# Optimization experiments

Measured on AMD Instinct MI355X. Metric: run time of the kernel, lower is better.

The kernel has to match this reference:

```python
import jax, jax.numpy as jnp
import numpy as np

B, S, EMB, HID, IMG, ATT, K, HL = 64, 512, 768, 512, 2048, 512, 6, 20


def setup_inputs() -> dict:
    key = jax.random.key(0)
    ks = jax.random.split(key, 14)
    u = lambda k, shape: jax.random.uniform(k, shape, jnp.float32, -0.1, 0.1)
    return {
        "representations": jax.random.normal(ks[0], (B, S, EMB), jnp.float32),
        "lengths": jax.random.randint(ks[1], (B,), 0, S),
        "separate_images": jax.random.normal(ks[2], (B, K, IMG), jnp.float32),
        "visual_context": jax.random.normal(ks[3], (B, K * IMG), jnp.float32),
        "prev_hist": jax.random.normal(ks[4], (B, K, HL, EMB), jnp.float32),
        "hist_counts": jax.random.randint(ks[5], (B, K), 0, HL + 1),
        "masks": jax.random.randint(ks[6], (B, S, 1), 0, 2).astype(bool),
        "W_sep": u(ks[7], (IMG, HID)), "b_sep": jnp.zeros((HID,), jnp.float32),
        "W_e2h": u(ks[8], (EMB, HID)), "b_e2h": jnp.zeros((HID,), jnp.float32),
        "W_hist": u(ks[9], (EMB, HID)), "b_hist": jnp.zeros((HID,), jnp.float32),
        "W_ctx": u(ks[10], (K * IMG, HID)), "b_ctx": jnp.zeros((HID,), jnp.float32),
        "W_mm": u(ks[11], (2 * HID, HID)), "b_mm": jnp.zeros((HID,), jnp.float32),
        "W_a1": u(ks[12], (HID, ATT)), "b_a1": jnp.zeros((ATT,), jnp.float32),
        "W_a2": u(ks[13], (ATT, 1)), "b_a2": jnp.zeros((1,), jnp.float32),
    }


def reference(representations, lengths, separate_images, visual_context,
              prev_hist, hist_counts, masks,
              W_sep, b_sep, W_e2h, b_e2h, W_hist, b_hist, W_ctx, b_ctx,
              W_mm, b_mm, W_a1, b_a1, W_a2, b_a2):
    # dropout_prob = 0 -> dropout is identity (eval-mode equivalence)
    input_reps = jax.nn.relu(representations @ W_e2h + b_e2h)          # [B,S,H]
    ctx = jax.nn.relu(visual_context @ W_ctx + b_ctx)                  # [B,H]
    ctx_rep = jnp.broadcast_to(ctx[:, None, :], input_reps.shape)
    mm = jax.nn.relu(jnp.concatenate([input_reps, ctx_rep], -1) @ W_mm + b_mm)  # [B,S,H]
    scores = jnp.tanh(mm @ W_a1 + b_a1) @ W_a2 + b_a2                  # [B,S,1]
    scores = jnp.where(masks, -jnp.inf, scores)
    att_w = jax.nn.softmax(scores, axis=1)                             # softmax over seq
    attended = jnp.sum(mm * att_w, axis=1)                             # [B,H]

    sep = separate_images @ W_sep + b_sep                              # [B,K,H]
    hl = prev_hist.shape[2]
    valid = jnp.arange(hl)[None, None, :] < hist_counts[:, :, None]    # [B,K,HL]
    hsum = jnp.sum(prev_hist * valid[..., None].astype(prev_hist.dtype), axis=2)
    havg = hsum / jnp.maximum(hist_counts, 1)[..., None].astype(prev_hist.dtype)
    hproj = jax.nn.relu(havg @ W_hist + b_hist)                        # [B,K,H]
    sep = sep + jnp.where((hist_counts > 0)[..., None], hproj, 0.0)
    sep = jax.nn.relu(sep)
    # F.normalize(p=2, dim=2, eps=1e-12)
    sep = sep / jnp.maximum(jnp.linalg.norm(sep, axis=2, keepdims=True), 1e-12)
    dot = jnp.einsum('bkh,bh->bk', sep, attended)[..., None]           # [B,K,1]
    return dot
```

## Files before the change

### kernel.cpp

```cpp
#include <hip/hip_runtime.h>
#include <math.h>

#define B_    64
#define S_    512
#define EMB_  768
#define HID_  512
#define IMG_  2048
#define ATT_  512
#define K_    6
#define HL_   20
#define MS_   (B_ * S_)

typedef __attribute__((ext_vector_type(8))) short bf16x8;
typedef __attribute__((ext_vector_type(4))) float f32x4;

__device__ __forceinline__ unsigned short f2b(float f) {
    unsigned int u = __float_as_uint(f);
    u += 0x7fffu + ((u >> 16) & 1u);
    return (unsigned short)(u >> 16);
}
__device__ __forceinline__ unsigned int pk_bf16(float lo, float hi) {
    unsigned int r;
    asm volatile("v_cvt_pk_bf16_f32 %0, %1, %2" : "=v"(r) : "v"(lo), "v"(hi));
    return r;
}

#define GLD_LDS16(gp, lp)                                                        \
    __builtin_amdgcn_global_load_lds(                                            \
        (const __attribute__((address_space(1))) void*)(gp),                     \
        (__attribute__((address_space(3))) void*)(lp), 16, 0, 0)

__global__ __launch_bounds__(256)
void prep(const float* __restrict__ W_e2h, const float* __restrict__ W_mm,
          const float* __restrict__ W_a1,
          unsigned short* __restrict__ WtE2H, unsigned short* __restrict__ WtMM,
          unsigned short* __restrict__ WtA1,
          const unsigned char* __restrict__ masks, int* __restrict__ flag) {
    const int z = blockIdx.z;
    if (z == 3) {
        if (blockIdx.x != 0 || blockIdx.y != 0) return;
        __shared__ int found;
        if (threadIdx.x == 0) found = 0;
        __syncthreads();
        for (int i = threadIdx.x; i < 8192; i += 256)
            if ((i & 3) != 0 && masks[i] != 0) found = 1;
        __syncthreads();
        if (threadIdx.x == 0) *flag = found;
        return;
    }
    const float* W;
    unsigned short* Wt;
    int Kd;
    if (z == 0)      { W = W_e2h; Wt = WtE2H; Kd = EMB_; }
    else if (z == 1) { W = W_mm;  Wt = WtMM;  Kd = HID_; }
    else             { W = W_a1;  Wt = WtA1;  Kd = HID_; }
    if ((int)blockIdx.x * 32 >= Kd) return;

    __shared__ float tile[32][33];
    int k0 = blockIdx.x * 32, n0 = blockIdx.y * 32;
    int tx = threadIdx.x & 31, ty = threadIdx.x >> 5;
    #pragma unroll
    for (int i = 0; i < 4; ++i)
        tile[ty + i * 8][tx] = W[(size_t)(k0 + ty + i * 8) * HID_ + n0 + tx];
    __syncthreads();
    #pragma unroll
    for (int i = 0; i < 4; ++i)
        Wt[(size_t)(n0 + ty + i * 8) * Kd + k0 + tx] = f2b(tile[tx][ty + i * 8]);
}

__device__ __forceinline__ void tile_coords(int N, int& bm, int& bn) {
    const int nwg = gridDim.x;
    const int cpx = nwg >> 3;
    const int lid = ((int)blockIdx.x & 7) * cpx + ((int)blockIdx.x >> 3);
    const int ntl = N >> 7;
    bn = (lid % ntl) << 7;
    bm = (lid / ntl) << 7;
}

template<bool AF32, int ACT, bool SCORE>
__global__ __launch_bounds__(256)
void gemm_pipe(const void* __restrict__ Av, const unsigned short* __restrict__ Bt,
               const float* __restrict__ bias, const float* __restrict__ row_add,
               int row_div, unsigned short* __restrict__ Co,
               const float* __restrict__ W_a2, float* __restrict__ scores8,
               int M, int N, int Kd) {
    __shared__ unsigned short Als[2][128 * 64];
    __shared__ unsigned short Bls[2][128 * 64];
    const int tid = threadIdx.x;
    int bm, bn; tile_coords(N, bm, bn);
    const int lane = tid & 63, wid = tid >> 6;
    const int wr = wid >> 1, wc = wid & 1;
    const int fr = lane & 15, hi = lane >> 4;

    const unsigned short* Ab = (const unsigned short*)Av;
    const float* Af = (const float*)Av;

    f32x4 acc[4][4] = {};
    int srow[4], lcol[4], scol[4];
    #pragma unroll
    for (int c = 0; c < 4; ++c) {
        int g = c * 256 + tid;
        srow[c] = g >> 3;
        lcol[c] = g & 7;
        scol[c] = lcol[c] ^ (srow[c] & 7);
    }

    float4 ra[8];

    auto stageA_lds = [&](int t, int buf) {
        #pragma unroll
        for (int c = 0; c < 4; ++c) {
            int g = c * 256 + tid;
            GLD_LDS16(Ab + (size_t)(bm + srow[c]) * Kd + t * 64 + scol[c] * 8,
                      &Als[buf][g * 8]);
        }
    };
    auto stageB_lds = [&](int t, int buf) {
        #pragma unroll
        for (int c = 0; c < 4; ++c) {
            int g = c * 256 + tid;
            GLD_LDS16(Bt + (size_t)(bn + srow[c]) * Kd + t * 64 + scol[c] * 8,
                      &Bls[buf][g * 8]);
        }
    };
    auto loadA_regs = [&](int t) {
        #pragma unroll
        for (int c = 0; c < 4; ++c) {
            const float* p = Af + (size_t)(bm + srow[c]) * Kd + t * 64 + lcol[c] * 8;
            ra[2 * c]     = *(const float4*)p;
            ra[2 * c + 1] = *(const float4*)(p + 4);
        }
    };
    auto writeA = [&](int buf) {
        #pragma unroll
        for (int c = 0; c < 4; ++c) {
            uint4 u;
            u.x = pk_bf16(ra[2*c].x,   ra[2*c].y);
            u.y = pk_bf16(ra[2*c].z,   ra[2*c].w);
            u.z = pk_bf16(ra[2*c+1].x, ra[2*c+1].y);
            u.w = pk_bf16(ra[2*c+1].z, ra[2*c+1].w);
            *(uint4*)&Als[buf][(srow[c] * 8 + scol[c]) * 8] = u;
        }
    };
    auto compute = [&](int buf) {
        #pragma unroll
        for (int kk = 0; kk < 2; ++kk) {
            bf16x8 af[4], bv[4];
            #pragma unroll
            for (int m = 0; m < 4; ++m) {
                int row = wr * 64 + m * 16 + fr;
                int sc = (kk * 4 + hi) ^ (fr & 7);
                af[m] = *(const bf16x8*)&Als[buf][row * 64 + sc * 8];
            }
            #pragma unroll
            for (int n = 0; n < 4; ++n) {
                int row = wc * 64 + n * 16 + fr;
                int sc = (kk * 4 + hi) ^ (fr & 7);
                bv[n] = *(const bf16x8*)&Bls[buf][row * 64 + sc * 8];
            }
            #pragma unroll
            for (int m = 0; m < 4; ++m)
                #pragma unroll
                for (int n = 0; n < 4; ++n)
                    acc[m][n] = __builtin_amdgcn_mfma_f32_16x16x32_bf16(af[m], bv[n], acc[m][n], 0, 0, 0);
        }
    };

    const int nt = Kd >> 6;

    if constexpr (AF32) {
        loadA_regs(0);
        stageB_lds(0, 0);
        writeA(0);
    } else {
        stageA_lds(0, 0);
        stageB_lds(0, 0);
    }

    for (int t = 0; t < nt; ++t) {
        const int buf = t & 1;
        const bool pf = (t + 1 < nt);
        if (pf) {
            if constexpr (AF32) {
                loadA_regs(t + 1);
                stageB_lds(t + 1, buf ^ 1);
            } else {
                stageA_lds(t + 1, buf ^ 1);
                stageB_lds(t + 1, buf ^ 1);
            }
        }
        __builtin_amdgcn_sched_barrier(0);
        if (pf) {
            if constexpr (AF32) asm volatile("s_waitcnt vmcnt(12)" ::: "memory");
            else                asm volatile("s_waitcnt vmcnt(8)"  ::: "memory");
        } else {
            asm volatile("s_waitcnt vmcnt(0)" ::: "memory");
        }
        __builtin_amdgcn_s_barrier();
        __builtin_amdgcn_sched_barrier(0);

        compute(buf);

        if constexpr (AF32) {
            if (pf) {
                writeA(buf ^ 1);
                asm volatile("s_waitcnt lgkmcnt(0)" ::: "memory");
            }
        }
        __builtin_amdgcn_sched_barrier(0);
        __builtin_amdgcn_s_barrier();
    }

    if (SCORE) {
        float ba[4], wa[4];
        #pragma unroll
        for (int n = 0; n < 4; ++n) {
            int col = bn + wc * 64 + n * 16 + fr;
            ba[n] = bias[col];
            wa[n] = W_a2[col];
        }
        const int slot = (bn >> 7) * 2 + wc;
        #pragma unroll
        for (int m = 0; m < 4; ++m) {
            #pragma unroll
            for (int r = 0; r < 4; ++r) {
                float p = 0.f;
                #pragma unroll
                for (int n = 0; n < 4; ++n)
                    p += tanhf(acc[m][n][r] + ba[n]) * wa[n];
                p += __shfl_xor(p, 1, 64);
                p += __shfl_xor(p, 2, 64);
                p += __shfl_xor(p, 4, 64);
                p += __shfl_xor(p, 8, 64);
                if (fr == 0)
                    scores8[(size_t)slot * M + bm + wr * 64 + m * 16 + hi * 4 + r] = p;
            }
        }
    } else {
        #pragma unroll
        for (int m = 0; m < 4; ++m) {
            #pragma unroll
            for (int n = 0; n < 4; ++n) {
                int col = bn + wc * 64 + n * 16 + fr;
                float badd = bias ? bias[col] : 0.f;
                #pragma unroll
                for (int r = 0; r < 4; ++r) {
                    int row = bm + wr * 64 + m * 16 + hi * 4 + r;
                    float x = acc[m][n][r] + badd;
                    if (row_add) x += row_add[(size_t)(row / row_div) * N + col];
                    if (ACT == 1) x = fmaxf(x, 0.f);
                    Co[(size_t)row * N + col] = f2b(x);
                }
            }
        }
    }
}

__global__ __launch_bounds__(256)
void gemm_splitk(const float* __restrict__ A, const float* __restrict__ W,
                 float* __restrict__ P, int M, int N, int Kd, int kps) {
    __shared__ float As[16][68];
    __shared__ float Ws[16][64];
    const int tid = threadIdx.x;
    const int bm = blockIdx.y * 64, bn = blockIdx.x * 64;
    const int ks = blockIdx.z;
    const int tx = tid & 15, ty = tid >> 4;
    const int arow = tid >> 2, akq = tid & 3;
    const int wk = tid >> 4, wnq = tid & 15;

    float acc[4][4] = {};
    const int kbeg = ks * kps, kend = kbeg + kps;

    for (int k0 = kbeg; k0 < kend; k0 += 16) {
        float4 av = *(const float4*)&A[(size_t)(bm + arow) * Kd + k0 + akq * 4];
        float4 wv = *(const float4*)&W[(size_t)(k0 + wk) * N + bn + wnq * 4];
        As[akq * 4 + 0][arow] = av.x;
        As[akq * 4 + 1][arow] = av.y;
        As[akq * 4 + 2][arow] = av.z;
        As[akq * 4 + 3][arow] = av.w;
        *(float4*)&Ws[wk][wnq * 4] = wv;
        __syncthreads();
        #pragma unroll
        for (int kk = 0; kk < 16; ++kk) {
            float4 a4 = *(const float4*)&As[kk][ty * 4];
            float4 b4 = *(const float4*)&Ws[kk][tx * 4];
            float a_[4] = {a4.x, a4.y, a4.z, a4.w};
            float b_[4] = {b4.x, b4.y, b4.z, b4.w};
            #pragma unroll
            for (int i = 0; i < 4; ++i)
                #pragma unroll
                for (int j = 0; j < 4; ++j)
                    acc[i][j] += a_[i] * b_[j];
        }
        __syncthreads();
    }

    float* Pbase = P + (size_t)ks * M * N;
    #pragma unroll
    for (int i = 0; i < 4; ++i) {
        int row = bm + ty * 4 + i;
        float4 v = {acc[i][0], acc[i][1], acc[i][2], acc[i][3]};
        *(float4*)&Pbase[(size_t)row * N + bn + tx * 4] = v;
    }
}

template<int ACT>
__global__ __launch_bounds__(256)
void reduce_k(const float* __restrict__ P, const float* __restrict__ bias,
              float* __restrict__ C, int MN, int N, int nsplit) {
    int idx = blockIdx.x * 256 + threadIdx.x;
    if (idx >= MN) return;
    float s = 0.f;
    for (int z = 0; z < nsplit; ++z) s += P[(size_t)z * MN + idx];
    if (bias) s += bias[idx & (N - 1)];
    if (ACT == 1) s = fmaxf(s, 0.f);
    C[idx] = s;
}

__global__ __launch_bounds__(256)
void softmax8(const float* __restrict__ scores8, const float* __restrict__ b_a2,
              const void* __restrict__ masks_raw, const int* __restrict__ flag,
              float* __restrict__ attw) {
    int b = blockIdx.x, tid = threadIdx.x;
    bool isb = (*flag) != 0;
    const unsigned char* mb = (const unsigned char*)masks_raw;
    const int* mi = (const int*)masks_raw;
    int lane = tid & 63, wv = tid >> 6;
    __shared__ float red[4], red2[4];
    float bias = b_a2[0];

    float m = -INFINITY;
    for (int s = tid; s < S_; s += 256) {
        int idx = b * S_ + s;
        float v = bias;
        #pragma unroll
        for (int z = 0; z < 8; ++z) v += scores8[(size_t)z * MS_ + idx];
        bool mk = isb ? (mb[idx] != 0) : (mi[idx] != 0);
        v = mk ? -INFINITY : v;
        attw[idx] = v;
        m = fmaxf(m, v);
    }
    #pragma unroll
    for (int off = 32; off; off >>= 1) m = fmaxf(m, __shfl_down(m, off, 64));
    if (lane == 0) red[wv] = m;
    __syncthreads();
    if (tid == 0) red[0] = fmaxf(fmaxf(red[0], red[1]), fmaxf(red[2], red[3]));
    __syncthreads();
    float Mx = red[0];

    float sum = 0.f;
    for (int s = tid; s < S_; s += 256) {
        int idx = b * S_ + s;
        float e = expf(attw[idx] - Mx);
        attw[idx] = e;
        sum += e;
    }
    #pragma unroll
    for (int off = 32; off; off >>= 1) sum += __shfl_down(sum, off, 64);
    if (lane == 0) red2[wv] = sum;
    __syncthreads();
    if (tid == 0) red2[0] = red2[0] + red2[1] + red2[2] + red2[3];
    __syncthreads();
    float inv = 1.f / red2[0];
    for (int s = tid; s < S_; s += 256) attw[b * S_ + s] *= inv;
}

__global__ __launch_bounds__(256)
void attended4(const unsigned short* __restrict__ mm, const float* __restrict__ attw,
               float* __restrict__ att4) {
    int b = blockIdx.x;
    int h = blockIdx.y * 256 + threadIdx.x;
    int z = blockIdx.z;
    __shared__ float w[128];
    int s0 = z * 128;
    if (threadIdx.x < 128) w[threadIdx.x] = attw[b * S_ + s0 + threadIdx.x];
    __syncthreads();
    float acc = 0.f;
    for (int s = 0; s < 128; ++s)
        acc += __uint_as_float((unsigned int)mm[((size_t)b * S_ + s0 + s) * HID_ + h] << 16) * w[s];
    att4[((size_t)z * B_ + b) * HID_ + h] = acc;
}

__global__ __launch_bounds__(256)
void hist_avg(const float* __restrict__ ph, const int* __restrict__ hcnt,
              float* __restrict__ havg) {
    int bk = blockIdx.x;
    int cnt = hcnt[bk];
    float denom = (float)(cnt > 1 ? cnt : 1);
    const float* base = ph + (size_t)bk * HL_ * EMB_;
    for (int e = threadIdx.x; e < EMB_; e += 256) {
        float s = 0.f;
        for (int l = 0; l < cnt; ++l) s += base[l * EMB_ + e];
        havg[bk * EMB_ + e] = s / denom;
    }
}

__global__ __launch_bounds__(256)
void combine_all(const float* __restrict__ skA, const float* __restrict__ skB,
                 const float* __restrict__ b_hist, const float* __restrict__ b_sep,
                 const int* __restrict__ hcnt, const float* __restrict__ att4,
                 float* __restrict__ out) {
    const int MNA = B_ * K_ * HID_;
    int bk = blockIdx.x, tid = threadIdx.x;
    int b = bk / K_;
    int cnt = hcnt[bk];
    float sq = 0.f, dt = 0.f;
    #pragma unroll
    for (int i = 0; i < HID_ / 256; ++i) {
        int h = tid + i * 256;
        size_t idx = (size_t)bk * HID_ + h;
        float hp = b_hist[h];
        #pragma unroll
        for (int z = 0; z < 8; ++z) hp += skA[(size_t)z * MNA + idx];
        hp = fmaxf(hp, 0.f);
        float sp = b_sep[h];
        #pragma unroll
        for (int z = 0; z < 16; ++z) sp += skB[(size_t)z * MNA + idx];
        float v = sp + (cnt > 0 ? hp : 0.f);
        v = fmaxf(v, 0.f);
        float at = 0.f;
        #pragma unroll
        for (int z = 0; z < 4; ++z) at += att4[((size_t)z * B_ + b) * HID_ + h];
        sq += v * v;
        dt += v * at;
    }
    #pragma unroll
    for (int off = 32; off; off >>= 1) {
        sq += __shfl_down(sq, off, 64);
        dt += __shfl_down(dt, off, 64);
    }
    __shared__ float rs[4], rd[4];
    int lane = tid & 63, wv = tid >> 6;
    if (lane == 0) { rs[wv] = sq; rd[wv] = dt; }
    __syncthreads();
    if (tid == 0) {
        float Sq = rs[0] + rs[1] + rs[2] + rs[3];
        float Dt = rd[0] + rd[1] + rd[2] + rd[3];
        float norm = fmaxf(sqrtf(Sq), 1e-12f);
        out[bk] = Dt / norm;
    }
}

extern "C" void kernel_launch(void* const* d_in, const int* in_sizes, int n_in,
                              void* d_out, int out_size, void* d_ws, size_t ws_size,
                              hipStream_t stream) {
    const float* reps     = (const float*)d_in[0];
    const float* sep_imgs = (const float*)d_in[2];
    const float* vctx     = (const float*)d_in[3];
    const float* phist    = (const float*)d_in[4];
    const int*   hcnt     = (const int*)d_in[5];
    const void*  masks    = d_in[6];
    const float* W_sep = (const float*)d_in[7];
    const float* b_sep = (const float*)d_in[8];
    const float* W_e2h = (const float*)d_in[9];
    const float* b_e2h = (const float*)d_in[10];
    const float* W_hist = (const float*)d_in[11];
    const float* b_hist = (const float*)d_in[12];
    const float* W_ctx = (const float*)d_in[13];
    const float* b_ctx = (const float*)d_in[14];
    const float* W_mm = (const float*)d_in[15];
    const float* b_mm = (const float*)d_in[16];
    const float* W_a1 = (const float*)d_in[17];
    const float* b_a1 = (const float*)d_in[18];
    const float* W_a2 = (const float*)d_in[19];
    const float* b_a2 = (const float*)d_in[20];
    float* out = (float*)d_out;

    const size_t MS = (size_t)MS_;
    const int MNA = B_ * K_ * HID_;

    unsigned short* actA  = (unsigned short*)d_ws;
    unsigned short* actB  = actA + MS * HID_;
    unsigned short* WtE2H = actB + MS * HID_;
    unsigned short* WtMM  = WtE2H + (size_t)EMB_ * HID_;
    unsigned short* WtA1  = WtMM + (size_t)HID_ * HID_;
    float* skC    = (float*)(WtA1 + (size_t)HID_ * HID_);
    float* skA    = skC + (size_t)64 * B_ * HID_;
    float* skB    = skA + (size_t)8 * MNA;
    float* scores8 = skB + (size_t)16 * MNA;
    float* attw   = scores8 + 8 * MS;
    float* att4   = attw + MS;
    float* ctx    = att4 + (size_t)4 * B_ * HID_;
    float* ctx2   = ctx + B_ * HID_;
    float* havg   = ctx2 + B_ * HID_;
    int*   flag   = (int*)(havg + (size_t)B_ * K_ * EMB_);

    prep<<<dim3(EMB_ / 32, HID_ / 32, 4), 256, 0, stream>>>(
        W_e2h, W_mm, W_a1, WtE2H, WtMM, WtA1, (const unsigned char*)masks, flag);

    {
        const int nsp = 64, kps = (K_ * IMG_) / nsp;
        gemm_splitk<<<dim3(8, 1, nsp), 256, 0, stream>>>(vctx, W_ctx, skC,
                                                         B_, HID_, K_ * IMG_, kps);
        reduce_k<1><<<(B_ * HID_ + 255) / 256, 256, 0, stream>>>(skC, b_ctx, ctx,
                                                                 B_ * HID_, HID_, nsp);
    }
    {
        const int nsp = 8, kps = HID_ / nsp;
        gemm_splitk<<<dim3(8, 1, nsp), 256, 0, stream>>>(ctx, W_mm + (size_t)HID_ * HID_,
                                                         skC, B_, HID_, HID_, kps);
        reduce_k<0><<<(B_ * HID_ + 255) / 256, 256, 0, stream>>>(skC, b_mm, ctx2,
                                                                 B_ * HID_, HID_, nsp);
    }

    const int big_grid = (MS_ / 128) * (HID_ / 128);
    gemm_pipe<true, 1, false><<<big_grid, 256, 0, stream>>>(
        reps, WtE2H, b_e2h, nullptr, 1, actA, nullptr, nullptr, MS_, HID_, EMB_);
    gemm_pipe<false, 1, false><<<big_grid, 256, 0, stream>>>(
        actA, WtMM, nullptr, ctx2, S_, actB, nullptr, nullptr, MS_, HID_, HID_);
    gemm_pipe<false, 0, true><<<big_grid, 256, 0, stream>>>(
        actB, WtA1, b_a1, nullptr, 1, actA, W_a2, scores8, MS_, ATT_, HID_);
    softmax8<<<B_, 256, 0, stream>>>(scores8, b_a2, masks, flag, attw);
    attended4<<<dim3(B_, HID_ / 256, 4), 256, 0, stream>>>(actB, attw, att4);
    hist_avg<<<B_ * K_, 256, 0, stream>>>(phist, hcnt, havg);
    gemm_splitk<<<dim3(8, 6, 8), 256, 0, stream>>>(havg, W_hist, skA,
                                                   B_ * K_, HID_, EMB_, EMB_ / 8);
    gemm_splitk<<<dim3(8, 6, 16), 256, 0, stream>>>(sep_imgs, W_sep, skB,
                                                    B_ * K_, HID_, IMG_, IMG_ / 16);
    combine_all<<<B_ * K_, 256, 0, stream>>>(skA, skB, b_hist, b_sep, hcnt,
                                             att4, out);
}
```

Before: 261.3 us.

## Halve GEMM K-tile, deepen fp32 A prefetch, raise occupancy, vectorize attended

The pipelined GEMM now uses a 32-wide K tile instead of 64, which halves LDS use and lets the kernel declare a minimum of 4 blocks per SM, with a 4-way XOR swizzle replacing the 8-way one. For the fp32-A path it adds a second register buffer so A is prefetched two K-steps ahead, and it raises MFMA wave priority during compute. The attended kernel is changed so each thread reads two packed bf16 values per load and writes a float2, which halves the grid. The trade-off is twice as many barrier and K-loop iterations, plus possible register pressure from the extra prefetch buffer under the occupancy bound.

```diff
diff --git a/kernel.cpp b/kernel.cpp
--- a/kernel.cpp
+++ b/kernel.cpp
@@ -24,6 +24,7 @@
     asm volatile("v_cvt_pk_bf16_f32 %0, %1, %2" : "=v"(r) : "v"(lo), "v"(hi));
     return r;
 }
+__device__ __forceinline__ int swz4(int r) { return (r ^ (r >> 2)) & 3; }
 
 #define GLD_LDS16(gp, lp)                                                        \
     __builtin_amdgcn_global_load_lds(                                            \
@@ -78,14 +79,14 @@
 }
 
 template<bool AF32, int ACT, bool SCORE>
-__global__ __launch_bounds__(256)
+__global__ __launch_bounds__(256, 4)
 void gemm_pipe(const void* __restrict__ Av, const unsigned short* __restrict__ Bt,
                const float* __restrict__ bias, const float* __restrict__ row_add,
                int row_div, unsigned short* __restrict__ Co,
                const float* __restrict__ W_a2, float* __restrict__ scores8,
                int M, int N, int Kd) {
-    __shared__ unsigned short Als[2][128 * 64];
-    __shared__ unsigned short Bls[2][128 * 64];
+    __shared__ unsigned short Als[2][128 * 32];
+    __shared__ unsigned short Bls[2][128 * 32];
     const int tid = threadIdx.x;
     int bm, bn; tile_coords(N, bm, bn);
     const int lane = tid & 63, wid = tid >> 6;
@@ -96,119 +97,120 @@
     const float* Af = (const float*)Av;
 
     f32x4 acc[4][4] = {};
-    int srow[4], lcol[4], scol[4];
-    #pragma unroll
-    for (int c = 0; c < 4; ++c) {
+    int srow[2], lin[2], scol[2];
+    #pragma unroll
+    for (int c = 0; c < 2; ++c) {
         int g = c * 256 + tid;
-        srow[c] = g >> 3;
-        lcol[c] = g & 7;
-        scol[c] = lcol[c] ^ (srow[c] & 7);
-    }
-
-    float4 ra[8];
+        srow[c] = g >> 2;
+        lin[c]  = g & 3;
+        scol[c] = lin[c] ^ swz4(srow[c]);
+    }
+
+    float4 raA[4], raB[4];
 
     auto stageA_lds = [&](int t, int buf) {
         #pragma unroll
-        for (int c = 0; c < 4; ++c) {
+        for (int c = 0; c < 2; ++c) {
             int g = c * 256 + tid;
-            GLD_LDS16(Ab + (size_t)(bm + srow[c]) * Kd + t * 64 + scol[c] * 8,
+            GLD_LDS16(Ab + (size_t)(bm + srow[c]) * Kd + t * 32 + scol[c] * 8,
                       &Als[buf][g * 8]);
         }
     };
     auto stageB_lds = [&](int t, int buf) {
         #pragma unroll
-        for (int c = 0; c < 4; ++c) {
+        for (int c = 0; c < 2; ++c) {
             int g = c * 256 + tid;
-            GLD_LDS16(Bt + (size_t)(bn + srow[c]) * Kd + t * 64 + scol[c] * 8,
+            GLD_LDS16(Bt + (size_t)(bn + srow[c]) * Kd + t * 32 + scol[c] * 8,
                       &Bls[buf][g * 8]);
         }
     };
-    auto loadA_regs = [&](int t) {
-        #pragma unroll
-        for (int c = 0; c < 4; ++c) {
-            const float* p = Af + (size_t)(bm + srow[c]) * Kd + t * 64 + lcol[c] * 8;
+    auto loadA = [&](int t, float4 (&ra)[4]) {
+        #pragma unroll
+        for (int c = 0; c < 2; ++c) {
+            const float* p = Af + (size_t)(bm + srow[c]) * Kd + t * 32 + scol[c] * 8;
             ra[2 * c]     = *(const float4*)p;
             ra[2 * c + 1] = *(const float4*)(p + 4);
         }
     };
-    auto writeA = [&](int buf) {
-        #pragma unroll
-        for (int c = 0; c < 4; ++c) {
+    auto writeA = [&](float4 (&ra)[4], int buf) {
+        #pragma unroll
+        for (int c = 0; c < 2; ++c) {
             uint4 u;
             u.x = pk_bf16(ra[2*c].x,   ra[2*c].y);
             u.y = pk_bf16(ra[2*c].z,   ra[2*c].w);
             u.z = pk_bf16(ra[2*c+1].x, ra[2*c+1].y);
             u.w = pk_bf16(ra[2*c+1].z, ra[2*c+1].w);
-            *(uint4*)&Als[buf][(srow[c] * 8 + scol[c]) * 8] = u;
+            *(uint4*)&Als[buf][(srow[c] * 4 + lin[c]) * 8] = u;
         }
     };
     auto compute = [&](int buf) {
-        #pragma unroll
-        for (int kk = 0; kk < 2; ++kk) {
-            bf16x8 af[4], bv[4];
+        bf16x8 af[4], bv[4];
+        #pragma unroll
+        for (int m = 0; m < 4; ++m) {
+            int r = wr * 64 + m * 16 + fr;
+            af[m] = *(const bf16x8*)&Als[buf][r * 32 + (hi ^ swz4(r)) * 8];
+        }
+        #pragma unroll
+        for (int n = 0; n < 4; ++n) {
+            int r = wc * 64 + n * 16 + fr;
+            bv[n] = *(const bf16x8*)&Bls[buf][r * 32 + (hi ^ swz4(r)) * 8];
+        }
+        __builtin_amdgcn_s_setprio(1);
+        #pragma unroll
+        for (int m = 0; m < 4; ++m)
             #pragma unroll
-            for (int m = 0; m < 4; ++m) {
-                int row = wr * 64 + m * 16 + fr;
-                int sc = (kk * 4 + hi) ^ (fr & 7);
-                af[m] = *(const bf16x8*)&Als[buf][row * 64 + sc * 8];
-            }
-            #pragma unroll
-            for (int n = 0; n < 4; ++n) {
-                int row = wc * 64 + n * 16 + fr;
-                int sc = (kk * 4 + hi) ^ (fr & 7);
-                bv[n] = *(const bf16x8*)&Bls[buf][row * 64 + sc * 8];
-            }
-            #pragma unroll
-            for (int m = 0; m < 4; ++m)
-                #pragma unroll
-                for (int n = 0; n < 4; ++n)
-                    acc[m][n] = __builtin_amdgcn_mfma_f32_16x16x32_bf16(af[m], bv[n], acc[m][n], 0, 0, 0);
-        }
+            for (int n = 0; n < 4; ++n)
+                acc[m][n] = __builtin_amdgcn_mfma_f32_16x16x32_bf16(af[m], bv[n], acc[m][n], 0, 0, 0);
+        __builtin_amdgcn_s_setprio(0);
     };
 
-    const int nt = Kd >> 6;
+    const int nt = Kd >> 5;
 
     if constexpr (AF32) {
-        loadA_regs(0);
+        loadA(0, raA);
         stageB_lds(0, 0);
-        writeA(0);
+        writeA(raA, 0);
+        loadA(1, raB);
     } else {
         stageA_lds(0, 0);
         stageB_lds(0, 0);
     }
 
-    for (int t = 0; t < nt; ++t) {
-        const int buf = t & 1;
-        const bool pf = (t + 1 < nt);
-        if (pf) {
-            if constexpr (AF32) {
-                loadA_regs(t + 1);
-                stageB_lds(t + 1, buf ^ 1);
-            } else {
-                stageA_lds(t + 1, buf ^ 1);
-                stageB_lds(t + 1, buf ^ 1);
-            }
-        }
+    auto phase = [&](int u, float4 (&raPF)[4], float4 (&raWR)[4],
+                     int bufU, int bufN) {
+        const bool pf1 = (u + 1 < nt);
+        const bool pf2 = (u + 2 < nt);
+        if constexpr (AF32) {
+            if (pf2) loadA(u + 2, raPF);
+        } else {
+            if (pf1) stageA_lds(u + 1, bufN);
+        }
+        if (pf1) stageB_lds(u + 1, bufN);
         __builtin_amdgcn_sched_barrier(0);
-        if (pf) {
-            if constexpr (AF32) asm volatile("s_waitcnt vmcnt(12)" ::: "memory");
-            else                asm volatile("s_waitcnt vmcnt(8)"  ::: "memory");
+        if constexpr (AF32) {
+            if (pf2)      asm volatile("s_waitcnt vmcnt(6)" ::: "memory");
+            else if (pf1) asm volatile("s_waitcnt vmcnt(2)" ::: "memory");
+            else          asm volatile("s_waitcnt vmcnt(0)" ::: "memory");
         } else {
-            asm volatile("s_waitcnt vmcnt(0)" ::: "memory");
+            if (pf1) asm volatile("s_waitcnt vmcnt(4)" ::: "memory");
+            else     asm volatile("s_waitcnt vmcnt(0)" ::: "memory");
         }
         __builtin_amdgcn_s_barrier();
         __builtin_amdgcn_sched_barrier(0);
-
-        compute(buf);
-
+        compute(bufU);
         if constexpr (AF32) {
-            if (pf) {
-                writeA(buf ^ 1);
+            if (pf1) {
+                writeA(raWR, bufN);
                 asm volatile("s_waitcnt lgkmcnt(0)" ::: "memory");
             }
         }
         __builtin_amdgcn_sched_barrier(0);
         __builtin_amdgcn_s_barrier();
+    };
+
+    for (int u = 0; u < nt; u += 2) {
+        phase(u,     raA, raB, 0, 1);
+        phase(u + 1, raB, raA, 1, 0);
     }
 
     if (SCORE) {
@@ -368,17 +370,22 @@
 __global__ __launch_bounds__(256)
 void attended4(const unsigned short* __restrict__ mm, const float* __restrict__ attw,
                float* __restrict__ att4) {
-    int b = blockIdx.x;
-    int h = blockIdx.y * 256 + threadIdx.x;
-    int z = blockIdx.z;
+    int b = blockIdx.x, z = blockIdx.y;
+    int h2 = threadIdx.x;
     __shared__ float w[128];
     int s0 = z * 128;
     if (threadIdx.x < 128) w[threadIdx.x] = attw[b * S_ + s0 + threadIdx.x];
     __syncthreads();
-    float acc = 0.f;
-    for (int s = 0; s < 128; ++s)
-        acc += __uint_as_float((unsigned int)mm[((size_t)b * S_ + s0 + s) * HID_ + h] << 16) * w[s];
-    att4[((size_t)z * B_ + b) * HID_ + h] = acc;
+    const unsigned int* base =
+        (const unsigned int*)mm + ((size_t)b * S_ + s0) * (HID_ / 2) + h2;
+    float a0 = 0.f, a1 = 0.f;
+    for (int s = 0; s < 128; ++s) {
+        unsigned int u = base[(size_t)s * (HID_ / 2)];
+        a0 += __uint_as_float(u << 16) * w[s];
+        a1 += __uint_as_float(u & 0xffff0000u) * w[s];
+    }
+    float2 r = {a0, a1};
+    *(float2*)&att4[((size_t)z * B_ + b) * HID_ + h2 * 2] = r;
 }
 
 __global__ __launch_bounds__(256)
@@ -511,7 +518,7 @@
     gemm_pipe<false, 0, true><<<big_grid, 256, 0, stream>>>(
         actB, WtA1, b_a1, nullptr, 1, actA, W_a2, scores8, MS_, ATT_, HID_);
     softmax8<<<B_, 256, 0, stream>>>(scores8, b_a2, masks, flag, attw);
-    attended4<<<dim3(B_, HID_ / 256, 4), 256, 0, stream>>>(actB, attw, att4);
+    attended4<<<dim3(B_, 4), 256, 0, stream>>>(actB, attw, att4);
     hist_avg<<<B_ * K_, 256, 0, stream>>>(phist, hcnt, havg);
     gemm_splitk<<<dim3(8, 6, 8), 256, 0, stream>>>(havg, W_hist, skA,
                                                    B_ * K_, HID_, EMB_, EMB_ / 8);
```

Result: slower. 359.4 us (+37.6%).

## Merge independent GEMMs into horizontally fused mega-kernels and vectorize attended reduction

Applied to the files above, without the earlier changes.

Independent work (the e2h GEMM, the context split-K GEMM, the history averaging and the separate-image split-K GEMM) now runs inside one launch that dispatches on block index, and the mm GEMM is merged the same way with the W_hist split-K. The aim is to cut launch count and fill idle compute units during small GEMMs. The pipelined GEMM loses its hand-tuned vmcnt waits and sched barriers in favor of plain __syncthreads, which may serialize the load/compute overlap. attended4 now reads two bf16 values per 32-bit load, with one block covering all 512 columns.

```diff
diff --git a/kernel.cpp b/kernel.cpp
--- a/kernel.cpp
+++ b/kernel.cpp
@@ -68,26 +68,26 @@
         Wt[(size_t)(n0 + ty + i * 8) * Kd + k0 + tx] = f2b(tile[tx][ty + i * 8]);
 }
 
-__device__ __forceinline__ void tile_coords(int N, int& bm, int& bn) {
-    const int nwg = gridDim.x;
+__device__ __forceinline__ void tile_coords(int bid, int nwg, int N, int& bm, int& bn) {
     const int cpx = nwg >> 3;
-    const int lid = ((int)blockIdx.x & 7) * cpx + ((int)blockIdx.x >> 3);
+    const int lid = (bid & 7) * cpx + (bid >> 3);
     const int ntl = N >> 7;
     bn = (lid % ntl) << 7;
     bm = (lid / ntl) << 7;
 }
 
 template<bool AF32, int ACT, bool SCORE>
-__global__ __launch_bounds__(256)
-void gemm_pipe(const void* __restrict__ Av, const unsigned short* __restrict__ Bt,
+__device__ __forceinline__
+void gemm_body(unsigned char* smem, int bid, int nwg,
+               const void* __restrict__ Av, const unsigned short* __restrict__ Bt,
                const float* __restrict__ bias, const float* __restrict__ row_add,
                int row_div, unsigned short* __restrict__ Co,
                const float* __restrict__ W_a2, float* __restrict__ scores8,
                int M, int N, int Kd) {
-    __shared__ unsigned short Als[2][128 * 64];
-    __shared__ unsigned short Bls[2][128 * 64];
+    unsigned short* Als = (unsigned short*)smem;
+    unsigned short* Bls = Als + 2 * 128 * 64;
     const int tid = threadIdx.x;
-    int bm, bn; tile_coords(N, bm, bn);
+    int bm, bn; tile_coords(bid, nwg, N, bm, bn);
     const int lane = tid & 63, wid = tid >> 6;
     const int wr = wid >> 1, wc = wid & 1;
     const int fr = lane & 15, hi = lane >> 4;
@@ -112,7 +112,7 @@
         for (int c = 0; c < 4; ++c) {
             int g = c * 256 + tid;
             GLD_LDS16(Ab + (size_t)(bm + srow[c]) * Kd + t * 64 + scol[c] * 8,
-                      &Als[buf][g * 8]);
+                      &Als[buf * 8192 + g * 8]);
         }
     };
     auto stageB_lds = [&](int t, int buf) {
@@ -120,10 +120,10 @@
         for (int c = 0; c < 4; ++c) {
             int g = c * 256 + tid;
             GLD_LDS16(Bt + (size_t)(bn + srow[c]) * Kd + t * 64 + scol[c] * 8,
-                      &Bls[buf][g * 8]);
+                      &Bls[buf * 8192 + g * 8]);
         }
     };
-    auto loadA_regs = [&](int t) {
+    auto loadA = [&](int t) {
         #pragma unroll
         for (int c = 0; c < 4; ++c) {
             const float* p = Af + (size_t)(bm + srow[c]) * Kd + t * 64 + lcol[c] * 8;
@@ -139,7 +139,7 @@
             u.y = pk_bf16(ra[2*c].z,   ra[2*c].w);
             u.z = pk_bf16(ra[2*c+1].x, ra[2*c+1].y);
             u.w = pk_bf16(ra[2*c+1].z, ra[2*c+1].w);
-            *(uint4*)&Als[buf][(srow[c] * 8 + scol[c]) * 8] = u;
+            *(uint4*)&Als[buf * 8192 + (srow[c] * 8 + scol[c]) * 8] = u;
         }
     };
     auto compute = [&](int buf) {
@@ -148,15 +148,15 @@
             bf16x8 af[4], bv[4];
             #pragma unroll
             for (int m = 0; m < 4; ++m) {
-                int row = wr * 64 + m * 16 + fr;
+                int r = wr * 64 + m * 16 + fr;
                 int sc = (kk * 4 + hi) ^ (fr & 7);
-                af[m] = *(const bf16x8*)&Als[buf][row * 64 + sc * 8];
+                af[m] = *(const bf16x8*)&Als[buf * 8192 + r * 64 + sc * 8];
             }
             #pragma unroll
             for (int n = 0; n < 4; ++n) {
-                int row = wc * 64 + n * 16 + fr;
+                int r = wc * 64 + n * 16 + fr;
                 int sc = (kk * 4 + hi) ^ (fr & 7);
-                bv[n] = *(const bf16x8*)&Bls[buf][row * 64 + sc * 8];
+                bv[n] = *(const bf16x8*)&Bls[buf * 8192 + r * 64 + sc * 8];
             }
             #pragma unroll
             for (int m = 0; m < 4; ++m)
@@ -169,46 +169,32 @@
     const int nt = Kd >> 6;
 
     if constexpr (AF32) {
-        loadA_regs(0);
+        loadA(0);
         stageB_lds(0, 0);
         writeA(0);
     } else {
         stageA_lds(0, 0);
         stageB_lds(0, 0);
     }
+    __syncthreads();
 
     for (int t = 0; t < nt; ++t) {
         const int buf = t & 1;
         const bool pf = (t + 1 < nt);
         if (pf) {
             if constexpr (AF32) {
-                loadA_regs(t + 1);
+                loadA(t + 1);
                 stageB_lds(t + 1, buf ^ 1);
             } else {
                 stageA_lds(t + 1, buf ^ 1);
                 stageB_lds(t + 1, buf ^ 1);
             }
         }
-        __builtin_amdgcn_sched_barrier(0);
-        if (pf) {
-            if constexpr (AF32) asm volatile("s_waitcnt vmcnt(12)" ::: "memory");
-            else                asm volatile("s_waitcnt vmcnt(8)"  ::: "memory");
-        } else {
-            asm volatile("s_waitcnt vmcnt(0)" ::: "memory");
-        }
-        __builtin_amdgcn_s_barrier();
-        __builtin_amdgcn_sched_barrier(0);
-
         compute(buf);
-
         if constexpr (AF32) {
-            if (pf) {
-                writeA(buf ^ 1);
-                asm volatile("s_waitcnt lgkmcnt(0)" ::: "memory");
-            }
-        }
-        __builtin_amdgcn_sched_barrier(0);
-        __builtin_amdgcn_s_barrier();
+            if (pf) writeA(buf ^ 1);
+        }
+        __syncthreads();
     }
 
     if (SCORE) {
@@ -256,20 +242,20 @@
     }
 }
 
-__global__ __launch_bounds__(256)
-void gemm_splitk(const float* __restrict__ A, const float* __restrict__ W,
+__device__ __forceinline__
+void splitk_body(unsigned char* smem, int bx, int by, int bz,
+                 const float* __restrict__ A, const float* __restrict__ W,
                  float* __restrict__ P, int M, int N, int Kd, int kps) {
-    __shared__ float As[16][68];
-    __shared__ float Ws[16][64];
+    float (*As)[68] = (float(*)[68])smem;
+    float (*Ws)[64] = (float(*)[64])(smem + 16 * 68 * 4);
     const int tid = threadIdx.x;
-    const int bm = blockIdx.y * 64, bn = blockIdx.x * 64;
-    const int ks = blockIdx.z;
+    const int bm = by * 64, bn = bx * 64;
     const int tx = tid & 15, ty = tid >> 4;
     const int arow = tid >> 2, akq = tid & 3;
     const int wk = tid >> 4, wnq = tid & 15;
 
     float acc[4][4] = {};
-    const int kbeg = ks * kps, kend = kbeg + kps;
+    const int kbeg = bz * kps, kend = kbeg + kps;
 
     for (int k0 = kbeg; k0 < kend; k0 += 16) {
         float4 av = *(const float4*)&A[(size_t)(bm + arow) * Kd + k0 + akq * 4];
@@ -295,13 +281,86 @@
         __syncthreads();
     }
 
-    float* Pbase = P + (size_t)ks * M * N;
+    float* Pbase = P + (size_t)bz * M * N;
     #pragma unroll
     for (int i = 0; i < 4; ++i) {
         int row = bm + ty * 4 + i;
         float4 v = {acc[i][0], acc[i][1], acc[i][2], acc[i][3]};
         *(float4*)&Pbase[(size_t)row * N + bn + tx * 4] = v;
     }
+}
+
+__device__ __forceinline__
+void hist_body(const float* __restrict__ ph, const int* __restrict__ hcnt,
+               float* __restrict__ havg, int bk) {
+    int cnt = hcnt[bk];
+    float denom = (float)(cnt > 1 ? cnt : 1);
+    const float* base = ph + (size_t)bk * HL_ * EMB_;
+    for (int e = threadIdx.x; e < EMB_; e += 256) {
+        float s = 0.f;
+        for (int l = 0; l < cnt; ++l) s += base[l * EMB_ + e];
+        havg[bk * EMB_ + e] = s / denom;
+    }
+}
+
+__global__ __launch_bounds__(256)
+void mega1(const float* __restrict__ reps, const unsigned short* __restrict__ WtE2H,
+           const float* __restrict__ b_e2h, unsigned short* __restrict__ actA,
+           const float* __restrict__ vctx, const float* __restrict__ W_ctx,
+           float* __restrict__ skC,
+           const float* __restrict__ phist, const int* __restrict__ hcnt,
+           float* __restrict__ havg,
+           const float* __restrict__ sep_imgs, const float* __restrict__ W_sep,
+           float* __restrict__ skB) {
+    __shared__ __align__(16) unsigned char smem[65536];
+    const int bid = blockIdx.x;
+    if (bid < 1024) {
+        gemm_body<true, 1, false>(smem, bid, 1024, reps, WtE2H, b_e2h, nullptr, 1,
+                                  actA, nullptr, nullptr, MS_, HID_, EMB_);
+    } else if (bid < 1536) {
+        int b = bid - 1024;
+        splitk_body(smem, b & 7, 0, b >> 3, vctx, W_ctx, skC, B_, HID_,
+                    K_ * IMG_, (K_ * IMG_) / 64);
+    } else if (bid < 1920) {
+        hist_body(phist, hcnt, havg, bid - 1536);
+    } else {
+        int b = bid - 1920;
+        splitk_body(smem, b & 7, (b >> 3) % 6, b / 48, sep_imgs, W_sep, skB,
+                    B_ * K_, HID_, IMG_, IMG_ / 16);
+    }
+}
+
+__global__ __launch_bounds__(256)
+void mega2(const unsigned short* __restrict__ actA, const unsigned short* __restrict__ WtMM,
+           const float* __restrict__ ctx2, unsigned short* __restrict__ actB,
+           const float* __restrict__ havg, const float* __restrict__ W_hist,
+           float* __restrict__ skA) {
+    __shared__ __align__(16) unsigned char smem[65536];
+    const int bid = blockIdx.x;
+    if (bid < 1024) {
+        gemm_body<false, 1, false>(smem, bid, 1024, actA, WtMM, nullptr, ctx2, S_,
+                                   actB, nullptr, nullptr, MS_, HID_, HID_);
+    } else {
+        int b = bid - 1024;
+        splitk_body(smem, b & 7, (b >> 3) % 6, b / 48, havg, W_hist, skA,
+                    B_ * K_, HID_, EMB_, EMB_ / 8);
+    }
+}
+
+__global__ __launch_bounds__(256)
+void gemm_score(const unsigned short* __restrict__ actB, const unsigned short* __restrict__ WtA1,
+                const float* __restrict__ b_a1, const float* __restrict__ W_a2,
+                float* __restrict__ scores8) {
+    __shared__ __align__(16) unsigned char smem[65536];
+    gemm_body<false, 0, true>(smem, blockIdx.x, 1024, actB, WtA1, b_a1, nullptr, 1,
+                              nullptr, W_a2, scores8, MS_, ATT_, HID_);
+}
+
+__global__ __launch_bounds__(256)
+void gemm_splitk(const float* __restrict__ A, const float* __restrict__ W,
+                 float* __restrict__ P, int M, int N, int Kd, int kps) {
+    __shared__ __align__(16) unsigned char smem[16 * 68 * 4 + 16 * 64 * 4];
+    splitk_body(smem, blockIdx.x, blockIdx.y, blockIdx.z, A, W, P, M, N, Kd, kps);
 }
 
 template<int ACT>
@@ -368,31 +427,22 @@
 __global__ __launch_bounds__(256)
 void attended4(const unsigned short* __restrict__ mm, const float* __restrict__ attw,
                float* __restrict__ att4) {
-    int b = blockIdx.x;
-    int h = blockIdx.y * 256 + threadIdx.x;
-    int z = blockIdx.z;
+    int b = blockIdx.x, z = blockIdx.y;
+    int h2 = threadIdx.x;
     __shared__ float w[128];
     int s0 = z * 128;
     if (threadIdx.x < 128) w[threadIdx.x] = attw[b * S_ + s0 + threadIdx.x];
     __syncthreads();
-    float acc = 0.f;
-    for (int s = 0; s < 128; ++s)
-        acc += __uint_as_float((unsigned int)mm[((size_t)b * S_ + s0 + s) * HID_ + h] << 16) * w[s];
-    att4[((size_t)z * B_ + b) * HID_ + h] = acc;
-}
-
-__global__ __launch_bounds__(256)
-void hist_avg(const float* __restrict__ ph, const int* __restrict__ hcnt,
-              float* __restrict__ havg) {
-    int bk = blockIdx.x;
-    int cnt = hcnt[bk];
-    float denom = (float)(cnt > 1 ? cnt : 1);
-    const float* base = ph + (size_t)bk * HL_ * EMB_;
-    for (int e = threadIdx.x; e < EMB_; e += 256) {
-        float s = 0.f;
-        for (int l = 0; l < cnt; ++l) s += base[l * EMB_ + e];
-        havg[bk * EMB_ + e] = s / denom;
-    }
+    const unsigned int* base =
+        (const unsigned int*)mm + ((size_t)b * S_ + s0) * (HID_ / 2) + h2;
+    float a0 = 0.f, a1 = 0.f;
+    for (int s = 0; s < 128; ++s) {
+        unsigned int u = base[(size_t)s * (HID_ / 2)];
+        a0 += __uint_as_float(u << 16) * w[s];
+        a1 += __uint_as_float(u & 0xffff0000u) * w[s];
+    }
+    float2 r = {a0, a1};
+    *(float2*)&att4[((size_t)z * B_ + b) * HID_ + h2 * 2] = r;
 }
 
 __global__ __launch_bounds__(256)
@@ -488,35 +538,24 @@
     prep<<<dim3(EMB_ / 32, HID_ / 32, 4), 256, 0, stream>>>(
         W_e2h, W_mm, W_a1, WtE2H, WtMM, WtA1, (const unsigned char*)masks, flag);
 
-    {
-        const int nsp = 64, kps = (K_ * IMG_) / nsp;
-        gemm_splitk<<<dim3(8, 1, nsp), 256, 0, stream>>>(vctx, W_ctx, skC,
-                                                         B_, HID_, K_ * IMG_, kps);
-        reduce_k<1><<<(B_ * HID_ + 255) / 256, 256, 0, stream>>>(skC, b_ctx, ctx,
-                                                                 B_ * HID_, HID_, nsp);
-    }
-    {
-        const int nsp = 8, kps = HID_ / nsp;
-        gemm_splitk<<<dim3(8, 1, nsp), 256, 0, stream>>>(ctx, W_mm + (size_t)HID_ * HID_,
-                                                         skC, B_, HID_, HID_, kps);
-        reduce_k<0><<<(B_ * HID_ + 255) / 256, 256, 0, stream>>>(skC, b_mm, ctx2,
-                                                                 B_ * HID_, HID_, nsp);
-    }
-
-    const int big_grid = (MS_ / 128) * (HID_ / 128);
-    gemm_pipe<true, 1, false><<<big_grid, 256, 0, stream>>>(
-        reps, WtE2H, b_e2h, nullptr, 1, actA, nullptr, nullptr, MS_, HID_, EMB_);
-    gemm_pipe<false, 1, false><<<big_grid, 256, 0, stream>>>(
-        actA, WtMM, nullptr, ctx2, S_, actB, nullptr, nullptr, MS_, HID_, HID_);
-    gemm_pipe<false, 0, true><<<big_grid, 256, 0, stream>>>(
-        actB, WtA1, b_a1, nullptr, 1, actA, W_a2, scores8, MS_, ATT_, HID_);
+    mega1<<<2688, 256, 0, stream>>>(reps, WtE2H, b_e2h, actA,
+                                    vctx, W_ctx, skC,
+                                    phist, hcnt, havg,
+                                    sep_imgs, W_sep, skB);
+
+    reduce_k<1><<<(B_ * HID_ + 255) / 256, 256, 0, stream>>>(skC, b_ctx, ctx,
+                                                             B_ * HID_, HID_, 64);
+    gemm_splitk<<<dim3(8, 1, 8), 256, 0, stream>>>(ctx, W_mm + (size_t)HID_ * HID_,
+                                                   skC, B_, HID_, HID_, HID_ / 8);
+    reduce_k<0><<<(B_ * HID_ + 255) / 256, 256, 0, stream>>>(skC, b_mm, ctx2,
+                                                             B_ * HID_, HID_, 8);
+
+    mega2<<<1408, 256, 0, stream>>>(actA, WtMM, ctx2, actB, havg, W_hist, skA);
+
+    gemm_score<<<1024, 256, 0, stream>>>(actB, WtA1, b_a1, W_a2, scores8);
+
     softmax8<<<B_, 256, 0, stream>>>(scores8, b_a2, masks, flag, attw);
-    attended4<<<dim3(B_, HID_ / 256, 4), 256, 0, stream>>>(actB, attw, att4);
-    hist_avg<<<B_ * K_, 256, 0, stream>>>(phist, hcnt, havg);
-    gemm_splitk<<<dim3(8, 6, 8), 256, 0, stream>>>(havg, W_hist, skA,
-                                                   B_ * K_, HID_, EMB_, EMB_ / 8);
-    gemm_splitk<<<dim3(8, 6, 16), 256, 0, stream>>>(sep_imgs, W_sep, skB,
-                                                    B_ * K_, HID_, IMG_, IMG_ / 16);
+    attended4<<<dim3(B_, 4), 256, 0, stream>>>(actB, attw, att4);
     combine_all<<<B_ * K_, 256, 0, stream>>>(skA, skB, b_hist, b_sep, hcnt,
                                              att4, out);
 }
```

After: 303.7 us. +16.2%, slower.

## Enlarge main GEMM tiles to 256x256 with 512 threads; vectorize attended reduction

Applied to the files above, without the earlier changes.

Replaces the 128x128, 256-thread pipelined bf16 MFMA GEMM with a 256x256 tile run by 512 threads (8 waves in a 2x4 layout, 8x4 accumulator fragments per wave). The aim is more operand reuse per LDS load and less global traffic per output. The hand-tuned vmcnt waits and split barriers are replaced by a plain __syncthreads per K-step. This uses 128KB of LDS per block and leaves only 256 blocks, about one per CU, so overlap between loading and compute could suffer. The attended4 kernel now loads two bf16 values per 32-bit access and stores float2 results, halving its thread count.

```diff
diff --git a/kernel.cpp b/kernel.cpp
--- a/kernel.cpp
+++ b/kernel.cpp
@@ -68,38 +68,37 @@
         Wt[(size_t)(n0 + ty + i * 8) * Kd + k0 + tx] = f2b(tile[tx][ty + i * 8]);
 }
 
-__device__ __forceinline__ void tile_coords(int N, int& bm, int& bn) {
+template<bool AF32, int ACT, bool SCORE>
+__global__ __launch_bounds__(512)
+void gemm256(const void* __restrict__ Av, const unsigned short* __restrict__ Bt,
+             const float* __restrict__ bias, const float* __restrict__ row_add,
+             int row_div, unsigned short* __restrict__ Co,
+             const float* __restrict__ W_a2, float* __restrict__ scores8,
+             int M, int N, int Kd) {
+    __shared__ unsigned short Als[2][256 * 64];
+    __shared__ unsigned short Bls[2][256 * 64];
+    const int tid = threadIdx.x;
+
     const int nwg = gridDim.x;
     const int cpx = nwg >> 3;
     const int lid = ((int)blockIdx.x & 7) * cpx + ((int)blockIdx.x >> 3);
-    const int ntl = N >> 7;
-    bn = (lid % ntl) << 7;
-    bm = (lid / ntl) << 7;
-}
-
-template<bool AF32, int ACT, bool SCORE>
-__global__ __launch_bounds__(256)
-void gemm_pipe(const void* __restrict__ Av, const unsigned short* __restrict__ Bt,
-               const float* __restrict__ bias, const float* __restrict__ row_add,
-               int row_div, unsigned short* __restrict__ Co,
-               const float* __restrict__ W_a2, float* __restrict__ scores8,
-               int M, int N, int Kd) {
-    __shared__ unsigned short Als[2][128 * 64];
-    __shared__ unsigned short Bls[2][128 * 64];
-    const int tid = threadIdx.x;
-    int bm, bn; tile_coords(N, bm, bn);
+    const int ntl = N >> 8;
+    const int bn = (lid % ntl) << 8;
+    const int bm = (lid / ntl) << 8;
+
     const int lane = tid & 63, wid = tid >> 6;
-    const int wr = wid >> 1, wc = wid & 1;
+    const int wr = wid >> 2, wc = wid & 3;
     const int fr = lane & 15, hi = lane >> 4;
 
     const unsigned short* Ab = (const unsigned short*)Av;
     const float* Af = (const float*)Av;
 
-    f32x4 acc[4][4] = {};
+    f32x4 acc[8][4] = {};
+
     int srow[4], lcol[4], scol[4];
     #pragma unroll
     for (int c = 0; c < 4; ++c) {
-        int g = c * 256 + tid;
+        int g = c * 512 + tid;
         srow[c] = g >> 3;
         lcol[c] = g & 7;
         scol[c] = lcol[c] ^ (srow[c] & 7);
@@ -110,7 +109,7 @@
     auto stageA_lds = [&](int t, int buf) {
         #pragma unroll
         for (int c = 0; c < 4; ++c) {
-            int g = c * 256 + tid;
+            int g = c * 512 + tid;
             GLD_LDS16(Ab + (size_t)(bm + srow[c]) * Kd + t * 64 + scol[c] * 8,
                       &Als[buf][g * 8]);
         }
@@ -118,15 +117,15 @@
     auto stageB_lds = [&](int t, int buf) {
         #pragma unroll
         for (int c = 0; c < 4; ++c) {
-            int g = c * 256 + tid;
+            int g = c * 512 + tid;
             GLD_LDS16(Bt + (size_t)(bn + srow[c]) * Kd + t * 64 + scol[c] * 8,
                       &Bls[buf][g * 8]);
         }
     };
-    auto loadA_regs = [&](int t) {
+    auto loadA = [&](int t) {
         #pragma unroll
         for (int c = 0; c < 4; ++c) {
-            const float* p = Af + (size_t)(bm + srow[c]) * Kd + t * 64 + lcol[c] * 8;
+            const float* p = Af + (size_t)(bm + srow[c]) * Kd + t * 64 + scol[c] * 8;
             ra[2 * c]     = *(const float4*)p;
             ra[2 * c + 1] = *(const float4*)(p + 4);
         }
@@ -134,32 +133,33 @@
     auto writeA = [&](int buf) {
         #pragma unroll
         for (int c = 0; c < 4; ++c) {
+            int g = c * 512 + tid;
             uint4 u;
             u.x = pk_bf16(ra[2*c].x,   ra[2*c].y);
             u.y = pk_bf16(ra[2*c].z,   ra[2*c].w);
             u.z = pk_bf16(ra[2*c+1].x, ra[2*c+1].y);
             u.w = pk_bf16(ra[2*c+1].z, ra[2*c+1].w);
-            *(uint4*)&Als[buf][(srow[c] * 8 + scol[c]) * 8] = u;
+            *(uint4*)&Als[buf][g * 8] = u;
         }
     };
     auto compute = [&](int buf) {
         #pragma unroll
         for (int kk = 0; kk < 2; ++kk) {
-            bf16x8 af[4], bv[4];
+            bf16x8 af[8], bv[4];
             #pragma unroll
-            for (int m = 0; m < 4; ++m) {
-                int row = wr * 64 + m * 16 + fr;
-                int sc = (kk * 4 + hi) ^ (fr & 7);
-                af[m] = *(const bf16x8*)&Als[buf][row * 64 + sc * 8];
+            for (int m = 0; m < 8; ++m) {
+                int r = wr * 128 + m * 16 + fr;
+                int sc = (kk * 4 + hi) ^ (r & 7);
+                af[m] = *(const bf16x8*)&Als[buf][r * 64 + sc * 8];
             }
             #pragma unroll
             for (int n = 0; n < 4; ++n) {
-                int row = wc * 64 + n * 16 + fr;
-                int sc = (kk * 4 + hi) ^ (fr & 7);
-                bv[n] = *(const bf16x8*)&Bls[buf][row * 64 + sc * 8];
+                int r = wc * 64 + n * 16 + fr;
+                int sc = (kk * 4 + hi) ^ (r & 7);
+                bv[n] = *(const bf16x8*)&Bls[buf][r * 64 + sc * 8];
             }
             #pragma unroll
-            for (int m = 0; m < 4; ++m)
+            for (int m = 0; m < 8; ++m)
                 #pragma unroll
                 for (int n = 0; n < 4; ++n)
                     acc[m][n] = __builtin_amdgcn_mfma_f32_16x16x32_bf16(af[m], bv[n], acc[m][n], 0, 0, 0);
@@ -169,46 +169,32 @@
     const int nt = Kd >> 6;
 
     if constexpr (AF32) {
-        loadA_regs(0);
+        loadA(0);
         stageB_lds(0, 0);
         writeA(0);
     } else {
         stageA_lds(0, 0);
         stageB_lds(0, 0);
     }
+    __syncthreads();
 
     for (int t = 0; t < nt; ++t) {
         const int buf = t & 1;
         const bool pf = (t + 1 < nt);
         if (pf) {
             if constexpr (AF32) {
-                loadA_regs(t + 1);
+                loadA(t + 1);
                 stageB_lds(t + 1, buf ^ 1);
             } else {
                 stageA_lds(t + 1, buf ^ 1);
                 stageB_lds(t + 1, buf ^ 1);
             }
         }
-        __builtin_amdgcn_sched_barrier(0);
-        if (pf) {
-            if constexpr (AF32) asm volatile("s_waitcnt vmcnt(12)" ::: "memory");
-            else                asm volatile("s_waitcnt vmcnt(8)"  ::: "memory");
-        } else {
-            asm volatile("s_waitcnt vmcnt(0)" ::: "memory");
-        }
-        __builtin_amdgcn_s_barrier();
-        __builtin_amdgcn_sched_barrier(0);
-
         compute(buf);
-
         if constexpr (AF32) {
-            if (pf) {
-                writeA(buf ^ 1);
-                asm volatile("s_waitcnt lgkmcnt(0)" ::: "memory");
-            }
-        }
-        __builtin_amdgcn_sched_barrier(0);
-        __builtin_amdgcn_s_barrier();
+            if (pf) writeA(buf ^ 1);
+        }
+        __syncthreads();
     }
 
     if (SCORE) {
@@ -219,9 +205,9 @@
             ba[n] = bias[col];
             wa[n] = W_a2[col];
         }
-        const int slot = (bn >> 7) * 2 + wc;
-        #pragma unroll
-        for (int m = 0; m < 4; ++m) {
+        const int slot = (bn >> 6) + wc;
+        #pragma unroll
+        for (int m = 0; m < 8; ++m) {
             #pragma unroll
             for (int r = 0; r < 4; ++r) {
                 float p = 0.f;
@@ -233,19 +219,19 @@
                 p += __shfl_xor(p, 4, 64);
                 p += __shfl_xor(p, 8, 64);
                 if (fr == 0)
-                    scores8[(size_t)slot * M + bm + wr * 64 + m * 16 + hi * 4 + r] = p;
+                    scores8[(size_t)slot * M + bm + wr * 128 + m * 16 + hi * 4 + r] = p;
             }
         }
     } else {
         #pragma unroll
-        for (int m = 0; m < 4; ++m) {
+        for (int m = 0; m < 8; ++m) {
             #pragma unroll
             for (int n = 0; n < 4; ++n) {
                 int col = bn + wc * 64 + n * 16 + fr;
                 float badd = bias ? bias[col] : 0.f;
                 #pragma unroll
                 for (int r = 0; r < 4; ++r) {
-                    int row = bm + wr * 64 + m * 16 + hi * 4 + r;
+                    int row = bm + wr * 128 + m * 16 + hi * 4 + r;
                     float x = acc[m][n][r] + badd;
                     if (row_add) x += row_add[(size_t)(row / row_div) * N + col];
                     if (ACT == 1) x = fmaxf(x, 0.f);
@@ -368,17 +354,22 @@
 __global__ __launch_bounds__(256)
 void attended4(const unsigned short* __restrict__ mm, const float* __restrict__ attw,
                float* __restrict__ att4) {
-    int b = blockIdx.x;
-    int h = blockIdx.y * 256 + threadIdx.x;
-    int z = blockIdx.z;
+    int b = blockIdx.x, z = blockIdx.y;
+    int h2 = threadIdx.x;
     __shared__ float w[128];
     int s0 = z * 128;
     if (threadIdx.x < 128) w[threadIdx.x] = attw[b * S_ + s0 + threadIdx.x];
     __syncthreads();
-    float acc = 0.f;
-    for (int s = 0; s < 128; ++s)
-        acc += __uint_as_float((unsigned int)mm[((size_t)b * S_ + s0 + s) * HID_ + h] << 16) * w[s];
-    att4[((size_t)z * B_ + b) * HID_ + h] = acc;
+    const unsigned int* base =
+        (const unsigned int*)mm + ((size_t)b * S_ + s0) * (HID_ / 2) + h2;
+    float a0 = 0.f, a1 = 0.f;
+    for (int s = 0; s < 128; ++s) {
+        unsigned int u = base[(size_t)s * (HID_ / 2)];
+        a0 += __uint_as_float(u << 16) * w[s];
+        a1 += __uint_as_float(u & 0xffff0000u) * w[s];
+    }
+    float2 r = {a0, a1};
+    *(float2*)&att4[((size_t)z * B_ + b) * HID_ + h2 * 2] = r;
 }
 
 __global__ __launch_bounds__(256)
@@ -503,15 +494,15 @@
                                                                  B_ * HID_, HID_, nsp);
     }
 
-    const int big_grid = (MS_ / 128) * (HID_ / 128);
-    gemm_pipe<true, 1, false><<<big_grid, 256, 0, stream>>>(
+    const int big_grid = (MS_ / 256) * (HID_ / 256);
+    gemm256<true, 1, false><<<big_grid, 512, 0, stream>>>(
         reps, WtE2H, b_e2h, nullptr, 1, actA, nullptr, nullptr, MS_, HID_, EMB_);
-    gemm_pipe<false, 1, false><<<big_grid, 256, 0, stream>>>(
+    gemm256<false, 1, false><<<big_grid, 512, 0, stream>>>(
         actA, WtMM, nullptr, ctx2, S_, actB, nullptr, nullptr, MS_, HID_, HID_);
-    gemm_pipe<false, 0, true><<<big_grid, 256, 0, stream>>>(
+    gemm256<false, 0, true><<<big_grid, 512, 0, stream>>>(
         actB, WtA1, b_a1, nullptr, 1, actA, W_a2, scores8, MS_, ATT_, HID_);
     softmax8<<<B_, 256, 0, stream>>>(scores8, b_a2, masks, flag, attw);
-    attended4<<<dim3(B_, HID_ / 256, 4), 256, 0, stream>>>(actB, attw, att4);
+    attended4<<<dim3(B_, 4), 256, 0, stream>>>(actB, attw, att4);
     hist_avg<<<B_ * K_, 256, 0, stream>>>(phist, hcnt, havg);
     gemm_splitk<<<dim3(8, 6, 8), 256, 0, stream>>>(havg, W_hist, skA,
                                                    B_ * K_, HID_, EMB_, EMB_ / 8);
```

Result: no change. 262.3 us (+0.4%).
